# Kernel tuning notes

Hardware: AMD Instinct MI355X
Metric: run time of the kernel (lower is better)

The kernel has to match this reference:

```python
import jax, jax.numpy as jnp
import numpy as np

EPS = 1e-6
NEG = -1e9

def rotate_half(x):
    x1, x2 = jnp.split(x, 2, axis=-1)
    return jnp.concatenate([-x2, x1], axis=-1)

def setup_inputs() -> dict:
    key = jax.random.key(0)
    ks = jax.random.split(key, 5)
    T, d_model, n_h = 2048, 2048, 16
    d_h = d_model // n_h
    x = jax.random.normal(ks[0], (T, d_model), dtype=jnp.float32)
    # RoPE tables (realistic rotary angles)
    inv_freq = 1.0 / (10000.0 ** (jnp.arange(0, d_h, 2, dtype=jnp.float32) / d_h))
    t = jnp.arange(T, dtype=jnp.float32)
    freqs = jnp.einsum('t,f->tf', t, inv_freq)
    emb = jnp.concatenate([freqs, freqs], axis=-1)  # [T, d_h]
    cos, sin = jnp.cos(emb), jnp.sin(emb)
    attention_mask = jnp.ones((T,), dtype=bool)
    ln_w = jnp.ones((d_model,), dtype=jnp.float32)
    w_qkv = jax.random.normal(ks[1], (3 * d_model, d_model), dtype=jnp.float32) / np.sqrt(d_model)
    w_o = jax.random.normal(ks[2], (d_model, d_model), dtype=jnp.float32) / np.sqrt(d_model)
    return {"x": x, "cos": cos, "sin": sin, "attention_mask": attention_mask,
            "ln_w": ln_w, "w_qkv": w_qkv, "w_o": w_o}

def reference(x, cos, sin, attention_mask, ln_w, w_qkv, w_o):
    T, d_model = x.shape
    n_h = 16
    d_h = d_model // n_h
    scale = 1.0 / np.sqrt(d_h)
    # RMSNorm
    ms = jnp.mean(x * x, axis=-1, keepdims=True)
    h = ln_w * x * jax.lax.rsqrt(ms + EPS)
    # fused QKV projection (eqx Linear: y = W @ x => h @ W.T)
    qkv = (h @ w_qkv.T).reshape(T, 3, n_h, d_h)
    q = qkv[:, 0].transpose(1, 0, 2)  # [H, T, d_h]
    k = qkv[:, 1].transpose(1, 0, 2)
    v = qkv[:, 2].transpose(1, 0, 2)
    # RoPE (cos/sin broadcast over heads)
    q = q * cos + rotate_half(q) * sin
    k = k * cos + rotate_half(k) * sin
    # attention scores with causal + padding mask
    scores = jnp.einsum('hqd,hkd->hqk', q, k) * scale
    causal = jnp.tril(jnp.ones((T, T), dtype=bool))[None]
    am = attention_mask.astype(bool)
    valid = causal & am[None, None, :]
    scores = jnp.where(valid, scores, NEG)
    scores = jnp.where(am[None, :, None], scores, NEG)
    probs = jax.nn.softmax(scores, axis=-1)
    out = jnp.einsum('hqk,hkd->hqd', probs, v)  # [H, T, d_h]
    out = out.transpose(1, 0, 2).reshape(T, d_model)
    out = out @ w_o.T
    out = jnp.where(attention_mask[:, None], out, 0.0)
    return x + out
```

## Files before the change

kernel.cpp:

```cpp
#include <hip/hip_runtime.h>


#define T_SEQ 2048
#define DM 2048
#define NH 16
#define DH 128
#define DM3 6144

typedef short s16x8 __attribute__((ext_vector_type(8)));
typedef float f32x4 __attribute__((ext_vector_type(4)));

static __device__ __forceinline__ unsigned short f2bf(float f){
  unsigned u = __builtin_bit_cast(unsigned, f);
  u += 0x7FFFu + ((u>>16)&1u);
  return (unsigned short)(u>>16);
}
static __device__ __forceinline__ float bf2f(unsigned short b){
  return __builtin_bit_cast(float, ((unsigned)b)<<16);
}
static __device__ __forceinline__ unsigned pk2bf(float a, float b){
  return (unsigned)f2bf(a) | ((unsigned)f2bf(b) << 16);
}
static __device__ __forceinline__ void gload_lds16(const void* g, void* l){
  __builtin_amdgcn_global_load_lds((const __attribute__((address_space(1))) void*)g,
                                   (__attribute__((address_space(3))) void*)l, 16, 0, 0);
}

__global__ __launch_bounds__(256) void cast_kernel(const float4* __restrict__ wq,
                                                   const float4* __restrict__ wo,
                                                   ushort4* __restrict__ wqo,
                                                   ushort4* __restrict__ woo,
                                                   int nq4, int ntot4){
  int i = blockIdx.x*256 + threadIdx.x;
  if (i >= ntot4) return;
  float4 v;
  if (i < nq4) v = wq[i]; else v = wo[i - nq4];
  ushort4 o; o.x=f2bf(v.x); o.y=f2bf(v.y); o.z=f2bf(v.z); o.w=f2bf(v.w);
  if (i < nq4) wqo[i] = o; else woo[i - nq4] = o;
}

__global__ __launch_bounds__(256) void rmsnorm_kernel(const float* __restrict__ x,
                                                      const float* __restrict__ w,
                                                      unsigned short* __restrict__ h){
  int row = blockIdx.x;
  int tid = threadIdx.x;
  const float4* xr = (const float4*)(x + (size_t)row*DM);
  float4 v0 = xr[tid], v1 = xr[tid+256];
  float ss = v0.x*v0.x+v0.y*v0.y+v0.z*v0.z+v0.w*v0.w
           + v1.x*v1.x+v1.y*v1.y+v1.z*v1.z+v1.w*v1.w;
  #pragma unroll
  for (int off=32; off; off>>=1) ss += __shfl_xor(ss, off, 64);
  __shared__ float wsum[4];
  if ((tid&63)==0) wsum[tid>>6] = ss;
  __syncthreads();
  float rs = rsqrtf((wsum[0]+wsum[1]+wsum[2]+wsum[3]) * (1.0f/DM) + 1e-6f);
  const float4* w4 = (const float4*)w;
  float4 wa = w4[tid], wb = w4[tid+256];
  ushort4* h4 = (ushort4*)(h + (size_t)row*DM);
  ushort4 o0, o1;
  o0.x=f2bf(v0.x*wa.x*rs); o0.y=f2bf(v0.y*wa.y*rs); o0.z=f2bf(v0.z*wa.z*rs); o0.w=f2bf(v0.w*wa.w*rs);
  o1.x=f2bf(v1.x*wb.x*rs); o1.y=f2bf(v1.y*wb.y*rs); o1.z=f2bf(v1.z*wb.z*rs); o1.w=f2bf(v1.w*wb.w*rs);
  h4[tid] = o0; h4[tid+256] = o1;
}

template <typename OUTT>
__global__ __launch_bounds__(256) void gemm_bt(const unsigned short* __restrict__ A,
                                               const unsigned short* __restrict__ B,
                                               OUTT* __restrict__ C,
                                               const float* __restrict__ resid,
                                               int M, int N, int K){
  __shared__ __align__(16) unsigned short As[128*32];
  __shared__ __align__(16) unsigned short Bs[128*32];
  int tid = threadIdx.x, lane = tid&63, wid = tid>>6;
  int c16 = lane&15, g = lane>>4;
  int bm = blockIdx.y, bn = blockIdx.x;
  int wr = wid>>1, wc = wid&1;
  f32x4 acc[4][4] = {};
  int nk = K >> 5;
  const char* Ab = (const char*)A;
  const char* Bb = (const char*)B;
  for (int ko=0; ko<nk; ++ko){
    #pragma unroll
    for (int c=0;c<2;c++){
      int li = (wid*2+c)*1024 + lane*16;
      int row = li>>6, colb = li&63;
      gload_lds16(Ab + ((size_t)(bm*128+row)*K + ko*32)*2 + colb,
                  (char*)As + (wid*2+c)*1024);
      gload_lds16(Bb + ((size_t)(bn*128+row)*K + ko*32)*2 + colb,
                  (char*)Bs + (wid*2+c)*1024);
    }
    __syncthreads();
    s16x8 af[4], bfr[4];
    #pragma unroll
    for (int m=0;m<4;m++) af[m]  = *(const s16x8*)&As[(wr*64+m*16+c16)*32 + g*8];
    #pragma unroll
    for (int n=0;n<4;n++) bfr[n] = *(const s16x8*)&Bs[(wc*64+n*16+c16)*32 + g*8];
    #pragma unroll
    for (int m=0;m<4;m++)
      #pragma unroll
      for (int n=0;n<4;n++)
        acc[m][n] = __builtin_amdgcn_mfma_f32_16x16x32_bf16(af[m], bfr[n], acc[m][n], 0,0,0);
    __syncthreads();
  }
  #pragma unroll
  for (int m=0;m<4;m++)
    #pragma unroll
    for (int n=0;n<4;n++){
      int r0 = bm*128 + wr*64 + m*16 + g*4;
      int c0 = bn*128 + wc*64 + n*16 + c16;
      #pragma unroll
      for (int r=0;r<4;r++){
        float v = acc[m][n][r];
        if (resid) v += resid[(size_t)(r0+r)*N + c0];
        if constexpr (__is_same(OUTT, float))
          C[(size_t)(r0+r)*N + c0] = v;
        else
          C[(size_t)(r0+r)*N + c0] = f2bf(v);
      }
    }
}

__global__ __launch_bounds__(256) void rope_kernel(const unsigned short* __restrict__ qkv,
                                                   const float* __restrict__ cs,
                                                   const float* __restrict__ sn,
                                                   unsigned short* __restrict__ Qr,
                                                   unsigned short* __restrict__ Kr){
  int idx = blockIdx.x*256 + threadIdx.x;
  int dh = idx & 63;
  int h  = (idx>>6) & (NH-1);
  int t  = idx >> 10;
  size_t base = (size_t)t*DM3 + h*DH;
  float c = cs[t*DH + dh], s = sn[t*DH + dh];
  float q1 = bf2f(qkv[base+dh]),      q2 = bf2f(qkv[base+dh+64]);
  float k1 = bf2f(qkv[base+DM+dh]),   k2 = bf2f(qkv[base+DM+dh+64]);
  const float sc = 0.088388347648318447f;
  size_t ob = ((size_t)h*T_SEQ + t)*DH + dh;
  Qr[ob]    = f2bf((q1*c - q2*s)*sc);
  Qr[ob+64] = f2bf((q2*c + q1*s)*sc);
  Kr[ob]    = f2bf(k1*c - k2*s);
  Kr[ob+64] = f2bf(k2*c + k1*s);
}

__global__ __launch_bounds__(256) void vtrans_kernel(const unsigned short* __restrict__ qkv,
                                                     unsigned short* __restrict__ Vt){
  __shared__ unsigned short tile[32][33];
  int t0 = blockIdx.x*32, d0 = blockIdx.y*32, h = blockIdx.z;
  int c = threadIdx.x & 31, r0 = threadIdx.x >> 5;
  #pragma unroll
  for (int i=0;i<4;i++){
    int r = r0 + i*8;
    tile[r][c] = qkv[(size_t)(t0+r)*DM3 + 2*DM + h*DH + d0 + c];
  }
  __syncthreads();
  #pragma unroll
  for (int i=0;i<4;i++){
    int d = r0 + i*8;
    Vt[((size_t)h*DH + d0 + d)*T_SEQ + t0 + c] = tile[c][d];
  }
}

__global__ __launch_bounds__(256) void attn_kernel(const unsigned short* __restrict__ Qr,
                                                   const unsigned short* __restrict__ Kr,
                                                   const unsigned short* __restrict__ Vt,
                                                   unsigned short* __restrict__ O){
  __shared__ float sm[4][16];
  __shared__ float sl[4][16];
  __shared__ __align__(16) unsigned short so[4][16][128];
  int tid = threadIdx.x;
  int lane = tid & 63, wid = tid >> 6;
  int c16 = lane & 15, g = lane >> 4;
  int id = blockIdx.x;
  int h  = id & 15;
  int qt = 127 - (id >> 4);
  int qr0 = qt * 16;
  const unsigned short* Qh = Qr + (size_t)h*T_SEQ*DH;
  const unsigned short* Kh = Kr + (size_t)h*T_SEQ*DH;
  const unsigned short* Vh = Vt + (size_t)h*DH*T_SEQ;
  s16x8 aq[4];
  #pragma unroll
  for (int kk=0;kk<4;kk++)
    aq[kk] = *(const s16x8*)&Qh[(size_t)(qr0+c16)*DH + kk*32 + g*8];
  f32x4 o[8] = {};
  float m_q = -1e30f, l_q = 0.f;
  int sig = 8*(c16>>2) + (c16&3);
  int nkv = (qr0 + 47) >> 5;
  int it0 = (wid*nkv) >> 2, it1 = ((wid+1)*nkv) >> 2;
  for (int it = it0; it < it1; ++it){
    int kv0 = it * 32;
    f32x4 sf[2] = {};
    #pragma unroll
    for (int n=0;n<2;n++)
      #pragma unroll
      for (int kk=0;kk<4;kk++){
        s16x8 bk = *(const s16x8*)&Kh[(size_t)(kv0 + sig + 4*n)*DH + kk*32 + g*8];
        sf[n] = __builtin_amdgcn_mfma_f32_16x16x32_bf16(bk, aq[kk], sf[n], 0,0,0);
      }
    if (kv0 + 31 > qr0){
      #pragma unroll
      for (int n=0;n<2;n++)
        #pragma unroll
        for (int r=0;r<4;r++)
          if (kv0 + 8*g + 4*n + r > qr0 + c16) sf[n][r] = -1e30f;
    }
    float mx = fmaxf(fmaxf(fmaxf(sf[0][0],sf[0][1]), fmaxf(sf[0][2],sf[0][3])),
                     fmaxf(fmaxf(sf[1][0],sf[1][1]), fmaxf(sf[1][2],sf[1][3])));
    mx = fmaxf(mx, __shfl_xor(mx, 16));
    mx = fmaxf(mx, __shfl_xor(mx, 32));
    float mnew = fmaxf(m_q, mx);
    float sc = __expf(m_q - mnew);
    m_q = mnew;
    float p[8];
    #pragma unroll
    for (int n=0;n<2;n++)
      #pragma unroll
      for (int r=0;r<4;r++) p[4*n+r] = __expf(sf[n][r] - mnew);
    float rs = ((p[0]+p[1])+(p[2]+p[3])) + ((p[4]+p[5])+(p[6]+p[7]));
    rs += __shfl_xor(rs, 16);
    rs += __shfl_xor(rs, 32);
    l_q = l_q*sc + rs;
    union { unsigned u[4]; s16x8 v; } pau;
    pau.u[0] = pk2bf(p[0],p[1]); pau.u[1] = pk2bf(p[2],p[3]);
    pau.u[2] = pk2bf(p[4],p[5]); pau.u[3] = pk2bf(p[6],p[7]);
    float scr[4];
    #pragma unroll
    for (int r=0;r<4;r++) scr[r] = __shfl(sc, g*4 + r);
    #pragma unroll
    for (int n2=0;n2<8;n2++)
      #pragma unroll
      for (int r=0;r<4;r++) o[n2][r] *= scr[r];
    #pragma unroll
    for (int n2=0;n2<8;n2++){
      s16x8 bv = *(const s16x8*)&Vh[(size_t)(n2*16+c16)*T_SEQ + kv0 + g*8];
      o[n2] = __builtin_amdgcn_mfma_f32_16x16x32_bf16(pau.v, bv, o[n2], 0,0,0);
    }
  }
  if (lane < 16){ sm[wid][lane] = m_q; sl[wid][lane] = l_q; }
  #pragma unroll
  for (int n2=0;n2<8;n2++)
    #pragma unroll
    for (int r=0;r<4;r++)
      so[wid][g*4+r][n2*16+c16] = f2bf(o[n2][r]);
  __syncthreads();
  int row = tid >> 4;
  int col = (tid & 15) * 8;
  float mg = fmaxf(fmaxf(sm[0][row], sm[1][row]), fmaxf(sm[2][row], sm[3][row]));
  float lg = 0.f;
  float acc[8] = {};
  #pragma unroll
  for (int w=0;w<4;w++){
    float e = __expf(sm[w][row] - mg);
    lg += sl[w][row] * e;
    #pragma unroll
    for (int j=0;j<8;j++) acc[j] += e * bf2f(so[w][row][col+j]);
  }
  float inv = 1.0f / lg;
  s16x8 ov;
  #pragma unroll
  for (int j=0;j<8;j++) ov[j] = (short)f2bf(acc[j]*inv);
  *(s16x8*)&O[(size_t)(qr0+row)*DM + h*DH + col] = ov;
}

extern "C" void kernel_launch(void* const* d_in, const int* in_sizes, int n_in,
                              void* d_out, int out_size, void* d_ws, size_t ws_size,
                              hipStream_t stream){
  const float* x    = (const float*)d_in[0];
  const float* cs   = (const float*)d_in[1];
  const float* sn   = (const float*)d_in[2];
  const float* ln_w = (const float*)d_in[4];
  const float* wqkv = (const float*)d_in[5];
  const float* wo   = (const float*)d_in[6];

  char* ws = (char*)d_ws;
  unsigned short* h     = (unsigned short*)(ws);
  unsigned short* wqkvb = (unsigned short*)(ws + 8388608);
  unsigned short* wob   = (unsigned short*)(ws + 33554432);
  unsigned short* qkv   = (unsigned short*)(ws + 41943040);
  unsigned short* attno = qkv;
  unsigned short* Qr    = (unsigned short*)(ws + 67108864);
  unsigned short* Kr    = (unsigned short*)(ws + 75497472);
  unsigned short* Vt    = (unsigned short*)(ws + 83886080);
  float* out            = (float*)d_out;

  cast_kernel<<<16384, 256, 0, stream>>>((const float4*)wqkv, (const float4*)wo,
                                         (ushort4*)wqkvb, (ushort4*)wob,
                                         3145728, 4194304);
  rmsnorm_kernel<<<2048, 256, 0, stream>>>(x, ln_w, h);
  gemm_bt<unsigned short><<<dim3(48,16), 256, 0, stream>>>(h, wqkvb, qkv, nullptr, 2048, 6144, 2048);
  rope_kernel<<<8192, 256, 0, stream>>>(qkv, cs, sn, Qr, Kr);
  vtrans_kernel<<<dim3(64,4,16), 256, 0, stream>>>(qkv, Vt);
  attn_kernel<<<dim3(2048), 256, 0, stream>>>(Qr, Kr, Vt, attno);
  gemm_bt<float><<<dim3(16,16), 256, 0, stream>>>(attno, wob, out, x, 2048, 2048, 2048);
}
```

Measured before the change: 390.1 us.

## Widen attention KV step to 64 and skip rescale when max grows little

The flash-attention inner loop now processes 64 KV columns per iteration instead of 32, so the max, exp-sum and rescale bookkeeping is paid once per 64 keys. It also adds a lazy rescaling threshold: the running max and the output rescale are updated only when some row's new max exceeds the old one by more than 8. This avoids many shuffles and multiplies on the output accumulator. The cost is higher register pressure, coarser splitting of causal work across waves, and exponent values up to e^8 before normalization.

Result: slower. 400.1 us (+2.6%).

```diff
diff --git a/kernel.cpp b/kernel.cpp
--- a/kernel.cpp
+++ b/kernel.cpp
@@ -183,55 +183,82 @@
   f32x4 o[8] = {};
   float m_q = -1e30f, l_q = 0.f;
   int sig = 8*(c16>>2) + (c16&3);
-  int nkv = (qr0 + 47) >> 5;
+  int nkv = (qr0 + 79) >> 6;
   int it0 = (wid*nkv) >> 2, it1 = ((wid+1)*nkv) >> 2;
   for (int it = it0; it < it1; ++it){
-    int kv0 = it * 32;
-    f32x4 sf[2] = {};
-    #pragma unroll
-    for (int n=0;n<2;n++)
-      #pragma unroll
-      for (int kk=0;kk<4;kk++){
-        s16x8 bk = *(const s16x8*)&Kh[(size_t)(kv0 + sig + 4*n)*DH + kk*32 + g*8];
-        sf[n] = __builtin_amdgcn_mfma_f32_16x16x32_bf16(bk, aq[kk], sf[n], 0,0,0);
-      }
-    if (kv0 + 31 > qr0){
+    int kv0 = it * 64;
+    f32x4 sf[2][2] = {};
+    #pragma unroll
+    for (int hf=0; hf<2; ++hf){
+      int kvh = kv0 + 32*hf;
       #pragma unroll
       for (int n=0;n<2;n++)
         #pragma unroll
-        for (int r=0;r<4;r++)
-          if (kv0 + 8*g + 4*n + r > qr0 + c16) sf[n][r] = -1e30f;
-    }
-    float mx = fmaxf(fmaxf(fmaxf(sf[0][0],sf[0][1]), fmaxf(sf[0][2],sf[0][3])),
-                     fmaxf(fmaxf(sf[1][0],sf[1][1]), fmaxf(sf[1][2],sf[1][3])));
+        for (int kk=0;kk<4;kk++){
+          s16x8 bk = *(const s16x8*)&Kh[(size_t)(kvh + sig + 4*n)*DH + kk*32 + g*8];
+          sf[hf][n] = __builtin_amdgcn_mfma_f32_16x16x32_bf16(bk, aq[kk], sf[hf][n], 0,0,0);
+        }
+    }
+    if (kv0 + 63 > qr0){
+      #pragma unroll
+      for (int hf=0; hf<2; ++hf)
+        #pragma unroll
+        for (int n=0;n<2;n++)
+          #pragma unroll
+          for (int r=0;r<4;r++)
+            if (kv0 + 32*hf + 8*g + 4*n + r > qr0 + c16) sf[hf][n][r] = -1e30f;
+    }
+    float mx = -1e30f;
+    #pragma unroll
+    for (int hf=0; hf<2; ++hf)
+      #pragma unroll
+      for (int n=0;n<2;n++)
+        #pragma unroll
+        for (int r=0;r<4;r++) mx = fmaxf(mx, sf[hf][n][r]);
     mx = fmaxf(mx, __shfl_xor(mx, 16));
     mx = fmaxf(mx, __shfl_xor(mx, 32));
-    float mnew = fmaxf(m_q, mx);
-    float sc = __expf(m_q - mnew);
-    m_q = mnew;
-    float p[8];
-    #pragma unroll
-    for (int n=0;n<2;n++)
-      #pragma unroll
-      for (int r=0;r<4;r++) p[4*n+r] = __expf(sf[n][r] - mnew);
-    float rs = ((p[0]+p[1])+(p[2]+p[3])) + ((p[4]+p[5])+(p[6]+p[7]));
+    if (!__all(mx - m_q <= 8.f)){
+      float mnew = fmaxf(m_q, mx);
+      float sc = __expf(m_q - mnew);
+      m_q = mnew;
+      float scr[4];
+      #pragma unroll
+      for (int r=0;r<4;r++) scr[r] = __shfl(sc, g*4 + r);
+      #pragma unroll
+      for (int n2=0;n2<8;n2++)
+        #pragma unroll
+        for (int r=0;r<4;r++) o[n2][r] *= scr[r];
+      l_q *= sc;
+    }
+    #pragma unroll
+    for (int hf=0; hf<2; ++hf)
+      #pragma unroll
+      for (int n=0;n<2;n++)
+        #pragma unroll
+        for (int r=0;r<4;r++) sf[hf][n][r] = __expf(sf[hf][n][r] - m_q);
+    float rs = 0.f;
+    #pragma unroll
+    for (int hf=0; hf<2; ++hf)
+      #pragma unroll
+      for (int n=0;n<2;n++)
+        #pragma unroll
+        for (int r=0;r<4;r++) rs += sf[hf][n][r];
     rs += __shfl_xor(rs, 16);
     rs += __shfl_xor(rs, 32);
-    l_q = l_q*sc + rs;
-    union { unsigned u[4]; s16x8 v; } pau;
-    pau.u[0] = pk2bf(p[0],p[1]); pau.u[1] = pk2bf(p[2],p[3]);
-    pau.u[2] = pk2bf(p[4],p[5]); pau.u[3] = pk2bf(p[6],p[7]);
-    float scr[4];
-    #pragma unroll
-    for (int r=0;r<4;r++) scr[r] = __shfl(sc, g*4 + r);
-    #pragma unroll
-    for (int n2=0;n2<8;n2++)
-      #pragma unroll
-      for (int r=0;r<4;r++) o[n2][r] *= scr[r];
-    #pragma unroll
-    for (int n2=0;n2<8;n2++){
-      s16x8 bv = *(const s16x8*)&Vh[(size_t)(n2*16+c16)*T_SEQ + kv0 + g*8];
-      o[n2] = __builtin_amdgcn_mfma_f32_16x16x32_bf16(pau.v, bv, o[n2], 0,0,0);
+    l_q += rs;
+    #pragma unroll
+    for (int hf=0; hf<2; ++hf){
+      union { unsigned u[4]; s16x8 v; } pau;
+      pau.u[0] = pk2bf(sf[hf][0][0], sf[hf][0][1]);
+      pau.u[1] = pk2bf(sf[hf][0][2], sf[hf][0][3]);
+      pau.u[2] = pk2bf(sf[hf][1][0], sf[hf][1][1]);
+      pau.u[3] = pk2bf(sf[hf][1][2], sf[hf][1][3]);
+      int kvh = kv0 + 32*hf;
+      #pragma unroll
+      for (int n2=0;n2<8;n2++){
+        s16x8 bv = *(const s16x8*)&Vh[(size_t)(n2*16+c16)*T_SEQ + kvh + g*8];
+        o[n2] = __builtin_amdgcn_mfma_f32_16x16x32_bf16(pau.v, bv, o[n2], 0,0,0);
+      }
     }
   }
   if (lane < 16){ sm[wid][lane] = m_q; sl[wid][lane] = l_q; }
```

## Pre-pack K and V into MFMA fragment order and skip unneeded softmax rescales

Applied to the files above, without the earlier changes.

The RoPE and V-transpose kernels now write K and V directly in per-lane MFMA operand order, so each attention lane loads one contiguous 16-byte chunk per fragment. This replaces strided row gathers with fully coalesced loads. The online softmax also rescales the output accumulators and running sum only when the new block max exceeds the stored max by more than 8, a lazy-rescale trick that saves exp and multiply work. The trade-off is unnormalised values up to e^8, which bf16 P and fp32 accumulators should tolerate.

Result: faster. 327.4 us (-16.1%).

```diff
diff --git a/kernel.cpp b/kernel.cpp
--- a/kernel.cpp
+++ b/kernel.cpp
@@ -6,6 +6,7 @@
 #define NH 16
 #define DH 128
 #define DM3 6144
+#define TD (T_SEQ*DH)
 
 typedef short s16x8 __attribute__((ext_vector_type(8)));
 typedef float f32x4 __attribute__((ext_vector_type(4)));
@@ -124,7 +125,7 @@
                                                    const float* __restrict__ cs,
                                                    const float* __restrict__ sn,
                                                    unsigned short* __restrict__ Qr,
-                                                   unsigned short* __restrict__ Kr){
+                                                   unsigned short* __restrict__ Kp){
   int idx = blockIdx.x*256 + threadIdx.x;
   int dh = idx & 63;
   int h  = (idx>>6) & (NH-1);
@@ -137,12 +138,20 @@
   size_t ob = ((size_t)h*T_SEQ + t)*DH + dh;
   Qr[ob]    = f2bf((q1*c - q2*s)*sc);
   Qr[ob+64] = f2bf((q2*c + q1*s)*sc);
-  Kr[ob]    = f2bf(k1*c - k2*s);
-  Kr[ob+64] = f2bf(k2*c + k1*s);
+  int b = t >> 5, r32 = t & 31;
+  int n   = (r32>>2) & 1;
+  int c16 = (r32&3) | ((r32>>3)<<2);
+  int g = (dh>>3)&3, e = dh&7;
+  int kk  = dh>>5;
+  int kk2 = 2 + kk;
+  size_t hb = (size_t)h*TD;
+  int slot = ((g*16+c16)<<3) + e;
+  Kp[hb + (size_t)((b*8 + n*4 + kk )*512 + slot)] = f2bf(k1*c - k2*s);
+  Kp[hb + (size_t)((b*8 + n*4 + kk2)*512 + slot)] = f2bf(k2*c + k1*s);
 }
 
 __global__ __launch_bounds__(256) void vtrans_kernel(const unsigned short* __restrict__ qkv,
-                                                     unsigned short* __restrict__ Vt){
+                                                     unsigned short* __restrict__ Vp){
   __shared__ unsigned short tile[32][33];
   int t0 = blockIdx.x*32, d0 = blockIdx.y*32, h = blockIdx.z;
   int c = threadIdx.x & 31, r0 = threadIdx.x >> 5;
@@ -152,16 +161,21 @@
     tile[r][c] = qkv[(size_t)(t0+r)*DM3 + 2*DM + h*DH + d0 + c];
   }
   __syncthreads();
-  #pragma unroll
-  for (int i=0;i<4;i++){
-    int d = r0 + i*8;
-    Vt[((size_t)h*DH + d0 + d)*T_SEQ + t0 + c] = tile[c][d];
+  int w = threadIdx.x;
+  if (w < 128){
+    int n2l = w>>6, lane = w&63;
+    int cc = lane&15, gg = lane>>4;
+    union { unsigned short u[8]; s16x8 v; } ov;
+    #pragma unroll
+    for (int e=0;e<8;e++) ov.u[e] = tile[gg*8+e][n2l*16+cc];
+    size_t dst = (size_t)h*TD + (size_t)(((t0>>5)*8 + (d0>>4) + n2l)*512 + lane*8);
+    *(s16x8*)&Vp[dst] = ov.v;
   }
 }
 
 __global__ __launch_bounds__(256) void attn_kernel(const unsigned short* __restrict__ Qr,
-                                                   const unsigned short* __restrict__ Kr,
-                                                   const unsigned short* __restrict__ Vt,
+                                                   const unsigned short* __restrict__ Kp,
+                                                   const unsigned short* __restrict__ Vp,
                                                    unsigned short* __restrict__ O){
   __shared__ float sm[4][16];
   __shared__ float sl[4][16];
@@ -173,26 +187,26 @@
   int h  = id & 15;
   int qt = 127 - (id >> 4);
   int qr0 = qt * 16;
-  const unsigned short* Qh = Qr + (size_t)h*T_SEQ*DH;
-  const unsigned short* Kh = Kr + (size_t)h*T_SEQ*DH;
-  const unsigned short* Vh = Vt + (size_t)h*DH*T_SEQ;
+  const unsigned short* Qh  = Qr + (size_t)h*TD;
+  const unsigned short* Kph = Kp + (size_t)h*TD;
+  const unsigned short* Vph = Vp + (size_t)h*TD;
   s16x8 aq[4];
   #pragma unroll
   for (int kk=0;kk<4;kk++)
     aq[kk] = *(const s16x8*)&Qh[(size_t)(qr0+c16)*DH + kk*32 + g*8];
   f32x4 o[8] = {};
   float m_q = -1e30f, l_q = 0.f;
-  int sig = 8*(c16>>2) + (c16&3);
   int nkv = (qr0 + 47) >> 5;
   int it0 = (wid*nkv) >> 2, it1 = ((wid+1)*nkv) >> 2;
   for (int it = it0; it < it1; ++it){
     int kv0 = it * 32;
+    int cb = it * 8;
     f32x4 sf[2] = {};
     #pragma unroll
     for (int n=0;n<2;n++)
       #pragma unroll
       for (int kk=0;kk<4;kk++){
-        s16x8 bk = *(const s16x8*)&Kh[(size_t)(kv0 + sig + 4*n)*DH + kk*32 + g*8];
+        s16x8 bk = *(const s16x8*)&Kph[(size_t)((cb + n*4 + kk)*512) + lane*8];
         sf[n] = __builtin_amdgcn_mfma_f32_16x16x32_bf16(bk, aq[kk], sf[n], 0,0,0);
       }
     if (kv0 + 31 > qr0){
@@ -206,31 +220,34 @@
                      fmaxf(fmaxf(sf[1][0],sf[1][1]), fmaxf(sf[1][2],sf[1][3])));
     mx = fmaxf(mx, __shfl_xor(mx, 16));
     mx = fmaxf(mx, __shfl_xor(mx, 32));
-    float mnew = fmaxf(m_q, mx);
-    float sc = __expf(m_q - mnew);
-    m_q = mnew;
+    if (!__all(mx - m_q <= 8.f)){
+      float mnew = fmaxf(m_q, mx);
+      float sc = __expf(m_q - mnew);
+      m_q = mnew;
+      float scr[4];
+      #pragma unroll
+      for (int r=0;r<4;r++) scr[r] = __shfl(sc, g*4 + r);
+      #pragma unroll
+      for (int n2=0;n2<8;n2++)
+        #pragma unroll
+        for (int r=0;r<4;r++) o[n2][r] *= scr[r];
+      l_q *= sc;
+    }
     float p[8];
     #pragma unroll
     for (int n=0;n<2;n++)
       #pragma unroll
-      for (int r=0;r<4;r++) p[4*n+r] = __expf(sf[n][r] - mnew);
+      for (int r=0;r<4;r++) p[4*n+r] = __expf(sf[n][r] - m_q);
     float rs = ((p[0]+p[1])+(p[2]+p[3])) + ((p[4]+p[5])+(p[6]+p[7]));
     rs += __shfl_xor(rs, 16);
     rs += __shfl_xor(rs, 32);
-    l_q = l_q*sc + rs;
+    l_q += rs;
     union { unsigned u[4]; s16x8 v; } pau;
     pau.u[0] = pk2bf(p[0],p[1]); pau.u[1] = pk2bf(p[2],p[3]);
     pau.u[2] = pk2bf(p[4],p[5]); pau.u[3] = pk2bf(p[6],p[7]);
-    float scr[4];
-    #pragma unroll
-    for (int r=0;r<4;r++) scr[r] = __shfl(sc, g*4 + r);
-    #pragma unroll
-    for (int n2=0;n2<8;n2++)
-      #pragma unroll
-      for (int r=0;r<4;r++) o[n2][r] *= scr[r];
     #pragma unroll
     for (int n2=0;n2<8;n2++){
-      s16x8 bv = *(const s16x8*)&Vh[(size_t)(n2*16+c16)*T_SEQ + kv0 + g*8];
+      s16x8 bv = *(const s16x8*)&Vph[(size_t)((cb + n2)*512) + lane*8];
       o[n2] = __builtin_amdgcn_mfma_f32_16x16x32_bf16(pau.v, bv, o[n2], 0,0,0);
     }
   }
@@ -277,8 +294,8 @@
   unsigned short* qkv   = (unsigned short*)(ws + 41943040);
   unsigned short* attno = qkv;
   unsigned short* Qr    = (unsigned short*)(ws + 67108864);
-  unsigned short* Kr    = (unsigned short*)(ws + 75497472);
-  unsigned short* Vt    = (unsigned short*)(ws + 83886080);
+  unsigned short* Kp    = (unsigned short*)(ws + 75497472);
+  unsigned short* Vp    = (unsigned short*)(ws + 83886080);
   float* out            = (float*)d_out;
 
   cast_kernel<<<16384, 256, 0, stream>>>((const float4*)wqkv, (const float4*)wo,
@@ -286,8 +303,8 @@
                                          3145728, 4194304);
   rmsnorm_kernel<<<2048, 256, 0, stream>>>(x, ln_w, h);
   gemm_bt<unsigned short><<<dim3(48,16), 256, 0, stream>>>(h, wqkvb, qkv, nullptr, 2048, 6144, 2048);
-  rope_kernel<<<8192, 256, 0, stream>>>(qkv, cs, sn, Qr, Kr);
-  vtrans_kernel<<<dim3(64,4,16), 256, 0, stream>>>(qkv, Vt);
-  attn_kernel<<<dim3(2048), 256, 0, stream>>>(Qr, Kr, Vt, attno);
+  rope_kernel<<<8192, 256, 0, stream>>>(qkv, cs, sn, Qr, Kp);
+  vtrans_kernel<<<dim3(64,4,16), 256, 0, stream>>>(qkv, Vp);
+  attn_kernel<<<dim3(2048), 256, 0, stream>>>(Qr, Kp, Vp, attno);
   gemm_bt<float><<<dim3(16,16), 256, 0, stream>>>(attno, wob, out, x, 2048, 2048, 2048);
 }
```
